# Optimization experiments

Hardware: AMD Instinct MI355X
Metric: run time of the kernel (lower is better)

## Reference

```python
import jax, jax.numpy as jnp
import numpy as np

BN_EPS = 1e-5


def conv1d(x, w, b, pad):
    # x: [N, Cin, L], w: [Cout, Cin, K], b: [Cout]
    out = jax.lax.conv_general_dilated(x, w, (1,), [(pad, pad)],
                                       dimension_numbers=("NCH", "OIH", "NCH"))
    return out + b[None, :, None]


def setup_inputs() -> dict:
    key = jax.random.key(0)
    ks = jax.random.split(key, 20)
    N, C, T, V = 64, 64, 256, 25
    S = 3                      # num_subset
    inter = C // 4             # inter_channels = out_channels // coff_embedding
    Cout = C
    ker_jpt = V if V % 2 else V - 1   # 25 -> spatial-attention kernel
    rr = 2

    x = jax.random.normal(ks[0], (N, C, T, V), dtype=jnp.float32)

    PA = 0.1 * jax.random.normal(ks[1], (S, V, V), dtype=jnp.float32)
    alpha = jnp.array([0.1], dtype=jnp.float32)
    Wa = 0.1 * jax.random.normal(ks[2], (S, inter, C), dtype=jnp.float32)
    ba = 0.01 * jax.random.normal(ks[3], (S, inter), dtype=jnp.float32)
    Wb = 0.1 * jax.random.normal(ks[4], (S, inter, C), dtype=jnp.float32)
    bb = 0.01 * jax.random.normal(ks[5], (S, inter), dtype=jnp.float32)
    Wd = 0.1 * jax.random.normal(ks[6], (S, Cout, C), dtype=jnp.float32)
    bd = 0.01 * jax.random.normal(ks[7], (S, Cout), dtype=jnp.float32)

    bn_gamma = 1.0 + 0.1 * jax.random.normal(ks[8], (Cout,), dtype=jnp.float32)
    bn_beta = 0.1 * jax.random.normal(ks[9], (Cout,), dtype=jnp.float32)

    Wsa = 0.05 * jax.random.normal(ks[10], (1, Cout, ker_jpt), dtype=jnp.float32)
    bsa = jnp.zeros((1,), dtype=jnp.float32)
    Wta = 0.05 * jax.random.normal(ks[11], (1, Cout, 9), dtype=jnp.float32)
    bta = jnp.zeros((1,), dtype=jnp.float32)

    W1 = 0.1 * jax.random.normal(ks[12], (Cout // rr, Cout), dtype=jnp.float32)
    b1 = jnp.zeros((Cout // rr,), dtype=jnp.float32)
    W2 = 0.1 * jax.random.normal(ks[13], (Cout, Cout // rr), dtype=jnp.float32)
    b2 = jnp.zeros((Cout,), dtype=jnp.float32)

    return dict(x=x, PA=PA, alpha=alpha, Wa=Wa, ba=ba, Wb=Wb, bb=bb, Wd=Wd, bd=bd,
                bn_gamma=bn_gamma, bn_beta=bn_beta, Wsa=Wsa, bsa=bsa, Wta=Wta,
                bta=bta, W1=W1, b1=b1, W2=W2, b2=b2)


def reference(x, PA, alpha, Wa, ba, Wb, bb, Wd, bd, bn_gamma, bn_beta,
              Wsa, bsa, Wta, bta, W1, b1, W2, b2):
    N, C, T, V = x.shape
    S, inter = Wa.shape[0], Wa.shape[1]
    denom = jnp.float32(inter * T)   # A1.size(-1) after view(N, V, inter*T)

    y = jnp.zeros((N, Wd.shape[1], T, V), dtype=x.dtype)
    for i in range(S):
        # 1x1 convs -> embeddings [N, inter, T, V]
        a = jnp.einsum("nctv,ic->nitv", x, Wa[i]) + ba[i][None, :, None, None]
        bf = jnp.einsum("nctv,ic->nitv", x, Wb[i]) + bb[i][None, :, None, None]
        # adaptive adjacency [N, V, V]
        A1 = jnp.tanh(jnp.einsum("nitv,nitw->nvw", a, bf) / denom)
        Ai = PA[i] + A1 * alpha[0]
        # graph aggregation + 1x1 conv_d
        z = jnp.einsum("nctv,nvw->nctw", x, Ai)
        y = y + jnp.einsum("nctv,oc->notv", z, Wd[i]) + bd[i][None, :, None, None]

    # eval-mode BatchNorm2d (running_mean=0, running_var=1)
    scale = bn_gamma / jnp.sqrt(1.0 + BN_EPS)
    y = y * scale[None, :, None, None] + bn_beta[None, :, None, None]
    # residual (in_channels == out_channels -> identity down)
    y = jax.nn.relu(y + x)

    # spatial SE gate: mean over T -> Conv1d over V
    se = y.mean(axis=2)                                   # [N, C, V]
    g = jax.nn.sigmoid(conv1d(se, Wsa, bsa, (Wsa.shape[-1] - 1) // 2))  # [N,1,V]
    y = y * g[:, :, None, :] + y

    # temporal SE gate: mean over V -> Conv1d over T
    se = y.mean(axis=3)                                   # [N, C, T]
    g = jax.nn.sigmoid(conv1d(se, Wta, bta, 4))           # [N, 1, T]
    y = y * g[:, :, :, None] + y

    # channel SE gate: global mean -> MLP
    se = y.mean(axis=(2, 3))                              # [N, C]
    h = jax.nn.relu(se @ W1.T + b1)
    g = jax.nn.sigmoid(h @ W2.T + b2)                     # [N, C]
    y = y * g[:, :, None, None] + y
    return y
```

## Files before the change

### kernel.cpp

```cpp
#include <hip/hip_runtime.h>
#include <math.h>


typedef __attribute__((ext_vector_type(8))) __bf16 bf16x8;
typedef __attribute__((ext_vector_type(4))) float  f32x4;

__global__ __launch_bounds__(256, 3) void gcn_kA(const float* __restrict__ x,
                                                 const float* __restrict__ Wa,
                                                 const float* __restrict__ ba,
                                                 const float* __restrict__ Wb,
                                                 const float* __restrict__ bb,
                                                 float* __restrict__ Pws) {
    const int bid = blockIdx.x;
    const int n  = bid >> 4;
    const int tt = bid & 15;
    const int tid  = threadIdx.x;
    const int lane = tid & 63;
    const int wv   = tid >> 6;
    const int col  = lane & 15;
    const int quad = lane >> 4;

    __shared__ __align__(16) __bf16 xB[112 * 72];
    __shared__ __align__(16) __bf16 aT[3][32 * 72];
    __shared__ __align__(16) __bf16 bT[3][32 * 72];

    for (int j = tid; j < 12 * 72; j += 256) xB[100 * 72 + j] = (__bf16)0.f;
    for (int j = tid; j < 7 * 72; j += 256) {
        #pragma unroll
        for (int s = 0; s < 3; ++s) {
            aT[s][25 * 72 + j] = (__bf16)0.f;
            bT[s][25 * 72 + j] = (__bf16)0.f;
        }
    }

    bf16x8 waf0[3], waf1[3], wbf0[3], wbf1[3];
    float ba4[3][4], bb4[3][4];
    #pragma unroll
    for (int s = 0; s < 3; ++s) {
        const float* wap = Wa + (size_t)s * 1024 + col * 64 + quad * 8;
        const float* wbp = Wb + (size_t)s * 1024 + col * 64 + quad * 8;
        #pragma unroll
        for (int j = 0; j < 8; ++j) { waf0[s][j] = (__bf16)wap[j];      wbf0[s][j] = (__bf16)wbp[j]; }
        #pragma unroll
        for (int j = 0; j < 8; ++j) { waf1[s][j] = (__bf16)wap[32 + j]; wbf1[s][j] = (__bf16)wbp[32 + j]; }
        #pragma unroll
        for (int r = 0; r < 4; ++r) {
            ba4[s][r] = ba[s * 16 + quad * 4 + r];
            bb4[s][r] = bb[s * 16 + quad * 4 + r];
        }
    }

    f32x4 pacc[3];
    #pragma unroll
    for (int s = 0; s < 3; ++s) pacc[s] = (f32x4){0.f, 0.f, 0.f, 0.f};
    const int mi = wv >> 1, ni = wv & 1;

    const float* xbase = x + (size_t)n * 409600 + tt * 400;

    for (int cc = 0; cc < 4; ++cc) {
        __syncthreads();
        const float* xc = xbase + cc * 100;
        #pragma unroll
        for (int it = 0; it < 7; ++it) {
            int j4 = tid + it * 256;
            if (j4 < 1600) {
                int c  = j4 / 25;
                int qq = (j4 - c * 25) * 4;
                float4 xv = *(const float4*)(xc + c * 6400 + qq);
                __bf16* dst = &xB[qq * 72 + c];
                dst[0]   = (__bf16)xv.x;
                dst[72]  = (__bf16)xv.y;
                dst[144] = (__bf16)xv.z;
                dst[216] = (__bf16)xv.w;
            }
        }
        __syncthreads();

        #pragma unroll
        for (int s = 0; s < 3; ++s) {
            for (int jt = wv; jt < 7; jt += 4) {
                int q = jt * 16 + col;
                const __bf16* bp = &xB[q * 72 + quad * 8];
                bf16x8 b0 = *(const bf16x8*)bp;
                bf16x8 b1 = *(const bf16x8*)(bp + 32);
                f32x4 da = {0.f, 0.f, 0.f, 0.f}, db = {0.f, 0.f, 0.f, 0.f};
                da = __builtin_amdgcn_mfma_f32_16x16x32_bf16(waf0[s], b0, da, 0, 0, 0);
                da = __builtin_amdgcn_mfma_f32_16x16x32_bf16(waf1[s], b1, da, 0, 0, 0);
                db = __builtin_amdgcn_mfma_f32_16x16x32_bf16(wbf0[s], b0, db, 0, 0, 0);
                db = __builtin_amdgcn_mfma_f32_16x16x32_bf16(wbf1[s], b1, db, 0, 0, 0);
                if (q < 100) {
                    int tl = q / 25, v = q - tl * 25;
                    #pragma unroll
                    for (int r = 0; r < 4; ++r) {
                        int k = (quad * 4 + r) * 4 + tl;
                        aT[s][v * 72 + k] = (__bf16)(da[r] + ba4[s][r]);
                        bT[s][v * 72 + k] = (__bf16)(db[r] + bb4[s][r]);
                    }
                }
            }
        }
        __syncthreads();

        #pragma unroll
        for (int s = 0; s < 3; ++s) {
            #pragma unroll
            for (int k0 = 0; k0 < 64; k0 += 32) {
                bf16x8 af  = *(const bf16x8*)&aT[s][(mi * 16 + col) * 72 + k0 + quad * 8];
                bf16x8 bfr = *(const bf16x8*)&bT[s][(ni * 16 + col) * 72 + k0 + quad * 8];
                pacc[s] = __builtin_amdgcn_mfma_f32_16x16x32_bf16(af, bfr, pacc[s], 0, 0, 0);
            }
        }
    }

    #pragma unroll
    for (int s = 0; s < 3; ++s) {
        #pragma unroll
        for (int r = 0; r < 4; ++r) {
            int v = mi * 16 + quad * 4 + r;
            int w = ni * 16 + col;
            if (v < 25 && w < 25)
                atomicAdd(&Pws[(size_t)(s * 64 + n) * 625 + v * 25 + w], pacc[s][r]);
        }
    }
}

__global__ __launch_bounds__(256) void gcn_kB(const float* __restrict__ Pws,
                                              const float* __restrict__ PA,
                                              const float* __restrict__ alpha,
                                              float* __restrict__ Ai) {
    int j = blockIdx.x * 256 + threadIdx.x;
    if (j < 120000) {
        int sn = j / 625;
        int r  = j - sn * 625;
        int s  = sn >> 6;
        Ai[j] = PA[s * 625 + r] + alpha[0] * tanhf(Pws[j] * (1.f / 4096.f));
    }
}

__global__ __launch_bounds__(256, 3) void gcn_kC(const float* __restrict__ x,
                                              const float* __restrict__ Ai,
                                              const float* __restrict__ Wd,
                                              const float* __restrict__ bd,
                                              const float* __restrict__ gamma,
                                              const float* __restrict__ beta,
                                              float* __restrict__ y1,
                                              float* __restrict__ meanT) {
    const int bid = blockIdx.x;
    const int tt = bid & 15;
    const int n  = bid >> 4;
    const int tid  = threadIdx.x;
    const int lane = tid & 63;
    const int wv   = tid >> 6;
    const int col  = lane & 15;
    const int quad = lane >> 4;

    __shared__ __align__(16) __bf16 xB[112 * 72];
    __shared__ __align__(16) __bf16 uL[256 * 40];

    for (int j = tid; j < 12 * 72; j += 256) xB[100 * 72 + j] = (__bf16)0.f;
    for (int j = tid; j < 256 * 15; j += 256) {
        int r = j / 15;
        int e = j - r * 15;
        uL[r * 40 + 25 + e] = (__bf16)0.f;
    }

    bf16x8 aiH[3][2], aiL[3][2];
    #pragma unroll
    for (int s = 0; s < 3; ++s) {
        #pragma unroll
        for (int vt = 0; vt < 2; ++vt) {
            int v = vt * 16 + col;
            #pragma unroll
            for (int j = 0; j < 8; ++j) {
                int w = quad * 8 + j;
                float val = (w < 25 && v < 25)
                          ? Ai[(size_t)(s * 64 + n) * 625 + w * 25 + v] : 0.f;
                __bf16 h = (__bf16)val;
                aiH[s][vt][j] = h;
                aiL[s][vt][j] = (__bf16)(val - (float)h);
            }
        }
    }

    bf16x8 wd0[3], wd1[3];
    #pragma unroll
    for (int s = 0; s < 3; ++s) {
        const float* wdp = Wd + (size_t)(s * 64 + wv * 16 + col) * 64 + quad * 8;
        #pragma unroll
        for (int j = 0; j < 8; ++j) wd0[s][j] = (__bf16)wdp[j];
        #pragma unroll
        for (int j = 0; j < 8; ++j) wd1[s][j] = (__bf16)wdp[32 + j];
    }

    float scv[4], btv[4], bdsv[4];
    #pragma unroll
    for (int ml = 0; ml < 4; ++ml) {
        int o = (wv * 4 + ml) * 4 + quad;
        scv[ml]  = gamma[o] * rsqrtf(1.f + 1e-5f);
        btv[ml]  = beta[o];
        bdsv[ml] = bd[o] + bd[64 + o] + bd[128 + o];
    }

    float msum[4][2];
    #pragma unroll
    for (int ml = 0; ml < 4; ++ml) { msum[ml][0] = 0.f; msum[ml][1] = 0.f; }

    const float* xbase = x + (size_t)n * 409600 + tt * 400;

    for (int cc = 0; cc < 4; ++cc) {
        f32x4 acc[4][2];
        #pragma unroll
        for (int ml = 0; ml < 4; ++ml) {
            acc[ml][0] = (f32x4){0.f, 0.f, 0.f, 0.f};
            acc[ml][1] = (f32x4){0.f, 0.f, 0.f, 0.f};
        }

        __syncthreads();
        const float* xc = xbase + cc * 100;
        #pragma unroll
        for (int it = 0; it < 7; ++it) {
            int j4 = tid + it * 256;
            if (j4 < 1600) {
                int c  = j4 / 25;
                int qq = (j4 - c * 25) * 4;
                float4 xv = *(const float4*)(xc + c * 6400 + qq);
                __bf16* dst = &xB[qq * 72 + c];
                dst[0]   = (__bf16)xv.x;
                dst[72]  = (__bf16)xv.y;
                dst[144] = (__bf16)xv.z;
                dst[216] = (__bf16)xv.w;
            }
        }
        __syncthreads();

        #pragma unroll
        for (int s = 0; s < 3; ++s) {
            #pragma unroll
            for (int qt = 0; qt < 7; ++qt) {
                const __bf16* bp = &xB[(qt * 16 + col) * 72 + quad * 8];
                bf16x8 b0 = *(const bf16x8*)bp;
                bf16x8 b1 = *(const bf16x8*)(bp + 32);
                f32x4 u = {0.f, 0.f, 0.f, 0.f};
                u = __builtin_amdgcn_mfma_f32_16x16x32_bf16(wd0[s], b0, u, 0, 0, 0);
                u = __builtin_amdgcn_mfma_f32_16x16x32_bf16(wd1[s], b1, u, 0, 0, 0);
                int q = qt * 16 + col;
                if (q < 100) {
                    int trel = q / 25, v = q - trel * 25;
                    int rowbase = ((wv * 16 + quad * 4) * 4 + trel) * 40 + v;
                    uL[rowbase]       = (__bf16)u[0];
                    uL[rowbase + 160] = (__bf16)u[1];
                    uL[rowbase + 320] = (__bf16)u[2];
                    uL[rowbase + 480] = (__bf16)u[3];
                }
            }
            #pragma unroll
            for (int ml = 0; ml < 4; ++ml) {
                int row = (wv * 4 + ml) * 16 + col;
                bf16x8 af = *(const bf16x8*)&uL[row * 40 + quad * 8];
                acc[ml][0] = __builtin_amdgcn_mfma_f32_16x16x32_bf16(af, aiH[s][0], acc[ml][0], 0, 0, 0);
                acc[ml][1] = __builtin_amdgcn_mfma_f32_16x16x32_bf16(af, aiH[s][1], acc[ml][1], 0, 0, 0);
                acc[ml][0] = __builtin_amdgcn_mfma_f32_16x16x32_bf16(af, aiL[s][0], acc[ml][0], 0, 0, 0);
                acc[ml][1] = __builtin_amdgcn_mfma_f32_16x16x32_bf16(af, aiL[s][1], acc[ml][1], 0, 0, 0);
            }
        }

        #pragma unroll
        for (int ml = 0; ml < 4; ++ml) {
            int o = (wv * 4 + ml) * 4 + quad;
            #pragma unroll
            for (int vt = 0; vt < 2; ++vt) {
                int v = vt * 16 + col;
                if (v < 25) {
                    const size_t base =
                        ((size_t)(n * 64 + o) * 256 + tt * 16 + cc * 4) * 25 + v;
                    float ms = 0.f;
                    #pragma unroll
                    for (int r = 0; r < 4; ++r) {
                        float val = scv[ml] * (acc[ml][vt][r] + bdsv[ml]) + btv[ml]
                                  + x[base + r * 25];
                        val = val > 0.f ? val : 0.f;
                        y1[base + r * 25] = val;
                        ms += val;
                    }
                    msum[ml][vt] += ms;
                }
            }
        }
    }

    #pragma unroll
    for (int ml = 0; ml < 4; ++ml) {
        int o = (wv * 4 + ml) * 4 + quad;
        #pragma unroll
        for (int vt = 0; vt < 2; ++vt) {
            int v = vt * 16 + col;
            if (v < 25)
                atomicAdd(&meanT[(n * 64 + o) * 25 + v], msum[ml][vt]);
        }
    }
}

__global__ __launch_bounds__(256) void gcn_kD(const float* __restrict__ meanT,
                                              const float* __restrict__ Wsa,
                                              const float* __restrict__ bsa,
                                              float* __restrict__ g2p) {
    const int n = blockIdx.x;
    const int tid = threadIdx.x;
    __shared__ float sm[1600], wl[1600];
    for (int j = tid; j < 1600; j += 256) {
        sm[j] = meanT[n * 1600 + j] * (1.f / 256.f);
        wl[j] = Wsa[j];
    }
    __syncthreads();
    if (tid < 25) {
        float acc = bsa[0];
        for (int c = 0; c < 64; ++c) {
            #pragma unroll
            for (int k = 0; k < 25; ++k) {
                int j = tid + k - 12;
                if (j >= 0 && j < 25) acc += sm[c * 25 + j] * wl[c * 25 + k];
            }
        }
        g2p[n * 25 + tid] = 1.f + 1.f / (1.f + expf(-acc));
    }
}

__global__ __launch_bounds__(256) void gcn_kE(const float* __restrict__ y1,
                                              const float* __restrict__ g2p,
                                              float* __restrict__ M2) {
    const int bid = blockIdx.x;
    const int n = bid >> 6;
    const int tid = threadIdx.x;
    __shared__ float yl[6400];
    __shared__ float g2l[25];
    const float* yp = y1 + (size_t)bid * 6400;
    for (int j = tid; j < 6400; j += 256) yl[j] = yp[j];
    if (tid < 25) g2l[tid] = g2p[n * 25 + tid];
    __syncthreads();
    float sum = 0.f;
    #pragma unroll
    for (int v = 0; v < 25; ++v) sum += yl[tid * 25 + v] * g2l[v];
    M2[bid * 256 + tid] = sum * 0.04f;
}

__global__ __launch_bounds__(256) void gcn_kFG(const float* __restrict__ M2,
                                               const float* __restrict__ Wta,
                                               const float* __restrict__ bta,
                                               const float* __restrict__ W1,
                                               const float* __restrict__ b1,
                                               const float* __restrict__ W2,
                                               const float* __restrict__ b2,
                                               float* __restrict__ g3p,
                                               float* __restrict__ g4p) {
    const int n = blockIdx.x;
    const int tid = threadIdx.x;
    __shared__ float m2L[64 * 260];
    __shared__ float wl[576];
    __shared__ float g3l[256], part[256], M3[64], h[32];

    for (int j = tid; j < 16384; j += 256) {
        int c = j >> 8, t = j & 255;
        m2L[c * 260 + t] = M2[(size_t)n * 16384 + j];
    }
    for (int j = tid; j < 576; j += 256) wl[j] = Wta[j];
    __syncthreads();

    {
        const int t = tid;
        float acc = bta[0];
        for (int c = 0; c < 64; ++c) {
            const float* mp = &m2L[c * 260];
            #pragma unroll
            for (int k = 0; k < 9; ++k) {
                int j = t + k - 4;
                if (j >= 0 && j < 256) acc += mp[j] * wl[c * 9 + k];
            }
        }
        float g3 = 1.f + 1.f / (1.f + expf(-acc));
        g3l[t] = g3;
        g3p[n * 256 + t] = g3;
    }
    __syncthreads();

    {
        const int c = tid >> 2, q = tid & 3;
        float p = 0.f;
        const float* mp = &m2L[c * 260 + q * 64];
        #pragma unroll 16
        for (int j = 0; j < 64; ++j) p += mp[j] * g3l[q * 64 + j];
        part[tid] = p;
    }
    __syncthreads();
    if (tid < 64)
        M3[tid] = (part[tid * 4] + part[tid * 4 + 1] + part[tid * 4 + 2] +
                   part[tid * 4 + 3]) * (1.f / 256.f);
    __syncthreads();
    if (tid < 32) {
        float acc = b1[tid];
        #pragma unroll 16
        for (int cc = 0; cc < 64; ++cc) acc += W1[tid * 64 + cc] * M3[cc];
        h[tid] = acc > 0.f ? acc : 0.f;
    }
    __syncthreads();
    if (tid < 64) {
        float acc = b2[tid];
        #pragma unroll
        for (int j = 0; j < 32; ++j) acc += W2[tid * 32 + j] * h[j];
        g4p[n * 64 + tid] = 1.f + 1.f / (1.f + expf(-acc));
    }
}

__global__ __launch_bounds__(256) void gcn_kH(float* __restrict__ y,
                                              const float* __restrict__ g2p,
                                              const float* __restrict__ g3p,
                                              const float* __restrict__ g4p) {
    const int bid = blockIdx.x;
    const int n = bid >> 6;
    const int tid = threadIdx.x;
    __shared__ float g3l[256], g2l[25];
    g3l[tid] = g3p[n * 256 + tid];
    if (tid < 25) g2l[tid] = g2p[n * 25 + tid];
    const float g4 = g4p[bid];
    __syncthreads();
    float4* yp = (float4*)(y + (size_t)bid * 6400);
    for (int f = tid; f < 1600; f += 256) {
        float4 val = yp[f];
        float* vv = (float*)&val;
        const int base = f * 4;
        #pragma unroll
        for (int k = 0; k < 4; ++k) {
            int idx = base + k;
            int t = (int)(((unsigned long long)idx * 1374389535ull) >> 35);
            int v = idx - t * 25;
            vv[k] *= g2l[v] * g3l[t] * g4;
        }
        yp[f] = val;
    }
}

extern "C" void kernel_launch(void* const* d_in, const int* in_sizes, int n_in,
                              void* d_out, int out_size, void* d_ws, size_t ws_size,
                              hipStream_t stream) {
    const float* x     = (const float*)d_in[0];
    const float* PA    = (const float*)d_in[1];
    const float* alpha = (const float*)d_in[2];
    const float* Wa    = (const float*)d_in[3];
    const float* ba    = (const float*)d_in[4];
    const float* Wb    = (const float*)d_in[5];
    const float* bb    = (const float*)d_in[6];
    const float* Wd    = (const float*)d_in[7];
    const float* bd    = (const float*)d_in[8];
    const float* gamma = (const float*)d_in[9];
    const float* beta  = (const float*)d_in[10];
    const float* Wsa   = (const float*)d_in[11];
    const float* bsa   = (const float*)d_in[12];
    const float* Wta   = (const float*)d_in[13];
    const float* bta   = (const float*)d_in[14];
    const float* W1    = (const float*)d_in[15];
    const float* b1    = (const float*)d_in[16];
    const float* W2    = (const float*)d_in[17];
    const float* b2    = (const float*)d_in[18];

    float* out = (float*)d_out;
    float* ws  = (float*)d_ws;

    float* Pws   = ws;
    float* Ai    = ws + 120000;
    float* meanT = ws + 252288;
    float* g2p   = ws + 354688;
    float* M2    = ws + 356288;
    float* g3p   = ws + 4550592;
    float* g4p   = ws + 4566976;

    hipMemsetAsync(Pws, 0, 120000 * sizeof(float), stream);
    hipMemsetAsync(meanT, 0, 102400 * sizeof(float), stream);

    gcn_kA<<<1024, 256, 0, stream>>>(x, Wa, ba, Wb, bb, Pws);
    gcn_kB<<<469, 256, 0, stream>>>(Pws, PA, alpha, Ai);
    gcn_kC<<<1024, 256, 0, stream>>>(x, Ai, Wd, bd, gamma, beta, out, meanT);
    gcn_kD<<<64, 256, 0, stream>>>(meanT, Wsa, bsa, g2p);
    gcn_kE<<<4096, 256, 0, stream>>>(out, g2p, M2);
    gcn_kFG<<<64, 256, 0, stream>>>(M2, Wta, bta, W1, b1, W2, b2, g3p, g4p);
    gcn_kH<<<4096, 256, 0, stream>>>(out, g2p, g3p, g4p);
}
```

Measured before the change: 607.9 us.

## Stage kC epilogue in per-wave LDS for vectorized residual/ReLU stores

The gcn_kC epilogue now writes the BN-scaled accumulator tile into a per-wave LDS buffer, which aliases the bf16 intermediate buffer. It then re-reads it in a row-contiguous order so the residual x load, ReLU and y1 store use 16-byte vector accesses instead of strided scalar ones. The per-(o,v) T-sums move from registers into an LDS array updated with shared-memory atomics and are flushed to meanT at the end. kE's y1 load is also vectorized to float4. The cost is extra LDS traffic and many LDS atomics, and correctness depends on intra-wave ordering of the aliased LDS reuse without barriers.

```diff
diff --git a/kernel.cpp b/kernel.cpp
--- a/kernel.cpp
+++ b/kernel.cpp
@@ -155,13 +155,18 @@
     const int quad = lane >> 4;
 
     __shared__ __align__(16) __bf16 xB[112 * 72];
-    __shared__ __align__(16) __bf16 uL[256 * 40];
+    __shared__ __align__(16) unsigned char uY[4 * 6656];
+    __shared__ float msumL[64 * 26];
+
+    __bf16* uLw = (__bf16*)(uY + wv * 6656);
+    float*  ySw = (float*) (uY + wv * 6656);
 
     for (int j = tid; j < 12 * 72; j += 256) xB[100 * 72 + j] = (__bf16)0.f;
-    for (int j = tid; j < 256 * 15; j += 256) {
-        int r = j / 15;
-        int e = j - r * 15;
-        uL[r * 40 + 25 + e] = (__bf16)0.f;
+    for (int j = tid; j < 64 * 26; j += 256) msumL[j] = 0.f;
+    {
+        __bf16* rz = uLw + lane * 40;
+        #pragma unroll
+        for (int k = 25; k < 32; ++k) rz[k] = (__bf16)0.f;
     }
 
     bf16x8 aiH[3][2], aiL[3][2];
@@ -201,11 +206,9 @@
         bdsv[ml] = bd[o] + bd[64 + o] + bd[128 + o];
     }
 
-    float msum[4][2];
-    #pragma unroll
-    for (int ml = 0; ml < 4; ++ml) { msum[ml][0] = 0.f; msum[ml][1] = 0.f; }
-
     const float* xbase = x + (size_t)n * 409600 + tt * 400;
+    const float* xgw   = x  + (size_t)(n * 64 + wv * 16) * 6400 + tt * 400;
+    float*       ygw   = y1 + (size_t)(n * 64 + wv * 16) * 6400 + tt * 400;
 
     for (int cc = 0; cc < 4; ++cc) {
         f32x4 acc[4][2];
@@ -246,17 +249,16 @@
                 int q = qt * 16 + col;
                 if (q < 100) {
                     int trel = q / 25, v = q - trel * 25;
-                    int rowbase = ((wv * 16 + quad * 4) * 4 + trel) * 40 + v;
-                    uL[rowbase]       = (__bf16)u[0];
-                    uL[rowbase + 160] = (__bf16)u[1];
-                    uL[rowbase + 320] = (__bf16)u[2];
-                    uL[rowbase + 480] = (__bf16)u[3];
+                    int rowbase = (quad * 16 + trel) * 40 + v;
+                    uLw[rowbase]       = (__bf16)u[0];
+                    uLw[rowbase + 160] = (__bf16)u[1];
+                    uLw[rowbase + 320] = (__bf16)u[2];
+                    uLw[rowbase + 480] = (__bf16)u[3];
                 }
             }
             #pragma unroll
             for (int ml = 0; ml < 4; ++ml) {
-                int row = (wv * 4 + ml) * 16 + col;
-                bf16x8 af = *(const bf16x8*)&uL[row * 40 + quad * 8];
+                bf16x8 af = *(const bf16x8*)&uLw[(ml * 16 + col) * 40 + quad * 8];
                 acc[ml][0] = __builtin_amdgcn_mfma_f32_16x16x32_bf16(af, aiH[s][0], acc[ml][0], 0, 0, 0);
                 acc[ml][1] = __builtin_amdgcn_mfma_f32_16x16x32_bf16(af, aiH[s][1], acc[ml][1], 0, 0, 0);
                 acc[ml][0] = __builtin_amdgcn_mfma_f32_16x16x32_bf16(af, aiL[s][0], acc[ml][0], 0, 0, 0);
@@ -266,36 +268,58 @@
 
         #pragma unroll
         for (int ml = 0; ml < 4; ++ml) {
-            int o = (wv * 4 + ml) * 4 + quad;
+            int ol = ml * 4 + quad;
             #pragma unroll
             for (int vt = 0; vt < 2; ++vt) {
                 int v = vt * 16 + col;
                 if (v < 25) {
-                    const size_t base =
-                        ((size_t)(n * 64 + o) * 256 + tt * 16 + cc * 4) * 25 + v;
-                    float ms = 0.f;
                     #pragma unroll
-                    for (int r = 0; r < 4; ++r) {
-                        float val = scv[ml] * (acc[ml][vt][r] + bdsv[ml]) + btv[ml]
-                                  + x[base + r * 25];
-                        val = val > 0.f ? val : 0.f;
-                        y1[base + r * 25] = val;
-                        ms += val;
-                    }
-                    msum[ml][vt] += ms;
+                    for (int r = 0; r < 4; ++r)
+                        ySw[ol * 104 + r * 25 + v] =
+                            scv[ml] * (acc[ml][vt][r] + bdsv[ml]) + btv[ml];
                 }
             }
         }
-    }
-
-    #pragma unroll
-    for (int ml = 0; ml < 4; ++ml) {
-        int o = (wv * 4 + ml) * 4 + quad;
-        #pragma unroll
-        for (int vt = 0; vt < 2; ++vt) {
-            int v = vt * 16 + col;
-            if (v < 25)
-                atomicAdd(&meanT[(n * 64 + o) * 25 + v], msum[ml][vt]);
+
+        const float* xc2 = xgw + cc * 100;
+        float*       yc2 = ygw + cc * 100;
+        #pragma unroll
+        for (int it = 0; it < 7; ++it) {
+            int j = lane + it * 64;
+            if (j < 400) {
+                int ol = j / 25, e = j - ol * 25;
+                f32x4 yp = *(const f32x4*)&ySw[ol * 104 + e * 4];
+                f32x4 xv = *(const f32x4*)(xc2 + ol * 6400 + e * 4);
+                f32x4 o4;
+                #pragma unroll
+                for (int k = 0; k < 4; ++k) {
+                    float val = yp[k] + xv[k];
+                    o4[k] = val > 0.f ? val : 0.f;
+                }
+                *(f32x4*)(yc2 + ol * 6400 + e * 4) = o4;
+                #pragma unroll
+                for (int k = 0; k < 4; ++k) {
+                    int q  = e * 4 + k;
+                    int v2 = q % 25;
+                    atomicAdd(&msumL[(wv * 16 + ol) * 26 + v2], o4[k]);
+                }
+            }
+        }
+
+        {
+            __bf16* rz = uLw + lane * 40;
+            #pragma unroll
+            for (int k = 25; k < 32; ++k) rz[k] = (__bf16)0.f;
+        }
+    }
+
+    #pragma unroll
+    for (int it = 0; it < 7; ++it) {
+        int j = lane + it * 64;
+        if (j < 400) {
+            int ol = j / 25, v = j - ol * 25;
+            atomicAdd(&meanT[(n * 64 + wv * 16 + ol) * 25 + v],
+                      msumL[(wv * 16 + ol) * 26 + v]);
         }
     }
 }
@@ -333,8 +357,9 @@
     const int tid = threadIdx.x;
     __shared__ float yl[6400];
     __shared__ float g2l[25];
-    const float* yp = y1 + (size_t)bid * 6400;
-    for (int j = tid; j < 6400; j += 256) yl[j] = yp[j];
+    const float4* yp = (const float4*)(y1 + (size_t)bid * 6400);
+    float4* ylv = (float4*)yl;
+    for (int j = tid; j < 1600; j += 256) ylv[j] = yp[j];
     if (tid < 25) g2l[tid] = g2p[n * 25 + tid];
     __syncthreads();
     float sum = 0.f;
```

New measurement: 679.1 us. 1.12x slower.
